# Optimization experiments

Measured on AMD Instinct MI355X. Metric: run time of the kernel, lower is better.

The kernel has to match this reference:

```python
import jax, jax.numpy as jnp
import numpy as np

N, E, F_IN, GCH, H, HID, NOUT, NG = 5000, 15000, 300, 2048, 4, 2048, 768, 128
NEG_SLOPE = 0.2


def gat_conv(x, W, att_src, att_dst, bias, src, dst):
    # x: [N, Fin]; W: [Fin, H*C]; att_*: [H, C]; bias: [H*C]
    n = x.shape[0]
    h = (x @ W).reshape(n, H, GCH)                      # [N,H,C]
    a_src = (h * att_src).sum(-1)                       # [N,H]
    a_dst = (h * att_dst).sum(-1)                       # [N,H]
    e = jax.nn.leaky_relu(a_src[src] + a_dst[dst], NEG_SLOPE)  # [E,H]
    m = jax.ops.segment_max(e, dst, num_segments=n)     # segment softmax over dst
    e = jnp.exp(e - m[dst])
    s = jax.ops.segment_sum(e, dst, num_segments=n)
    alpha = e / (s[dst] + 1e-16)                        # [E,H]
    msg = h[src] * alpha[:, :, None]                    # [E,H,C]
    out = jax.ops.segment_sum(msg, dst, num_segments=n) # [N,H,C]
    return out.reshape(n, H * GCH) + bias


def setup_inputs() -> dict:
    key = jax.random.key(0)
    ks = jax.random.split(key, 32)
    d = {}
    d['x'] = jax.random.normal(ks[0], (N, F_IN), jnp.float32)
    d['edge_index'] = jax.random.randint(ks[1], (2, E), 0, N, jnp.int32)
    d['batch'] = jnp.sort(jax.random.randint(ks[2], (N,), 0, NG, jnp.int32))
    dims_in = [F_IN, HID, HID]
    i = 3
    for l, fin in enumerate(dims_in, 1):
        sc = 1.0 / np.sqrt(fin)
        d[f'W{l}'] = jax.random.normal(ks[i], (fin, H * GCH), jnp.float32) * sc; i += 1
        d[f'asrc{l}'] = jax.random.normal(ks[i], (H, GCH), jnp.float32) * 0.02; i += 1
        d[f'adst{l}'] = jax.random.normal(ks[i], (H, GCH), jnp.float32) * 0.02; i += 1
        d[f'bc{l}'] = jnp.zeros((H * GCH,), jnp.float32)
        d[f'Wh{l}'] = jax.random.normal(ks[i], (H * GCH, HID), jnp.float32) * (1.0 / np.sqrt(H * GCH)); i += 1
        d[f'bh{l}'] = jnp.zeros((HID,), jnp.float32)
    d['Wm1'] = jax.random.normal(ks[i], (GCH, 2048), jnp.float32) * (1.0 / np.sqrt(GCH)); i += 1
    d['bm1'] = jnp.zeros((2048,), jnp.float32)
    d['Wm2'] = jax.random.normal(ks[i], (2048, NOUT), jnp.float32) * (1.0 / np.sqrt(2048)); i += 1
    d['bm2'] = jnp.zeros((NOUT,), jnp.float32)
    d['ln_g'] = jnp.ones((NOUT,), jnp.float32)
    d['ln_b'] = jnp.zeros((NOUT,), jnp.float32)
    return d


def reference(x, edge_index, batch,
              W1, asrc1, adst1, bc1, Wh1, bh1,
              W2, asrc2, adst2, bc2, Wh2, bh2,
              W3, asrc3, adst3, bc3, Wh3, bh3,
              Wm1, bm1, Wm2, bm2, ln_g, ln_b):
    n = x.shape[0]
    # PyG GATConv adds self-loops by default
    loops = jnp.arange(n, dtype=edge_index.dtype)
    src = jnp.concatenate([edge_index[0], loops])
    dst = jnp.concatenate([edge_index[1], loops])

    h = gat_conv(x, W1, asrc1, adst1, bc1, src, dst)
    h = jax.nn.relu(h @ Wh1 + bh1)
    h = gat_conv(h, W2, asrc2, adst2, bc2, src, dst)
    h = jax.nn.relu(h @ Wh2 + bh2)
    h = gat_conv(h, W3, asrc3, adst3, bc3, src, dst)
    h = h @ Wh3 + bh3                                   # no relu after head_linear3

    # global mean pool over graphs
    sums = jax.ops.segment_sum(h, batch, num_segments=NG)
    cnt = jax.ops.segment_sum(jnp.ones((n,), h.dtype), batch, num_segments=NG)
    g = sums / jnp.maximum(cnt, 1.0)[:, None]           # [NG, 2048]

    g = jax.nn.relu(g @ Wm1 + bm1)
    g = g @ Wm2 + bm2                                   # [NG, NOUT]
    mu = g.mean(-1, keepdims=True)
    var = ((g - mu) ** 2).mean(-1, keepdims=True)
    return (g - mu) / jnp.sqrt(var + 1e-5) * ln_g + ln_b
```

## Files before the change

kernel.cpp:

```cpp
#include <hip/hip_runtime.h>

typedef unsigned short u16;
typedef __attribute__((ext_vector_type(8))) short short8;
typedef __attribute__((ext_vector_type(4))) short s16x4;
typedef __attribute__((ext_vector_type(4))) float f32x4;

__device__ inline u16 f2bf(float f){
  unsigned int u = __builtin_bit_cast(unsigned int, f);
  u += 0x7fffu + ((u >> 16) & 1u);
  return (u16)(u >> 16);
}
__device__ inline float bf2f(u16 h){
  unsigned int u = ((unsigned int)h) << 16;
  return __builtin_bit_cast(float, u);
}

typedef __attribute__((address_space(1))) const void* as1_t;
typedef __attribute__((address_space(3))) void* as3_t;
__device__ __forceinline__ void gload16(const u16* g, u16* l) {
  __builtin_amdgcn_global_load_lds((as1_t)g, (as3_t)l, 16, 0, 0);
}

#define BARRIER() asm volatile("s_barrier" ::: "memory")
#define VMCNT4()  asm volatile("s_waitcnt vmcnt(4)" ::: "memory")
#define VMCNT0()  asm volatile("s_waitcnt vmcnt(0)" ::: "memory")
#define LGKM0()   asm volatile("s_waitcnt lgkmcnt(0)" ::: "memory")

__device__ __forceinline__ void gemm_core(
    const u16* __restrict__ A, const u16* __restrict__ B, u16* __restrict__ C,
    int tile_m, int tile_n, int abase, int hoff,
    int M, int K, int lda, int ldb, int ldc, u16* lds)
{
  int tid = threadIdx.x, wave = tid >> 6, lane = tid & 63;
  int wm = wave >> 2, wn = wave & 3;
  int NT = K >> 6;

  const u16* sA[2]; const u16* sB[2];
  int dq[2];
#pragma unroll
  for (int q = 0; q < 2; ++q) {
    int row = q * 128 + (tid >> 2);
    int cg  = (tid & 3) ^ ((row >> 1) & 3);
    sA[q] = A + (size_t)(abase + row) * lda + hoff + cg * 8;
    sB[q] = B + (size_t)(tile_n + row) * ldb + hoff + cg * 8;
    dq[q] = q * 4096 + tid * 8;
  }

  int l15 = lane & 15, c4 = lane >> 4;
  int aoff[8], boff[4];
#pragma unroll
  for (int mi = 0; mi < 8; ++mi) {
    int r = wm * 128 + mi * 16 + l15;
    aoff[mi] = r * 32 + ((c4 ^ ((r >> 1) & 3)) * 8);
  }
#pragma unroll
  for (int ni = 0; ni < 4; ++ni) {
    int r = wn * 64 + ni * 16 + l15;
    boff[ni] = r * 32 + ((c4 ^ ((r >> 1) & 3)) * 8);
  }

  f32x4 acc[8][4];
#pragma unroll
  for (int mi = 0; mi < 8; ++mi)
#pragma unroll
    for (int ni = 0; ni < 4; ++ni) { f32x4 z = {0.f,0.f,0.f,0.f}; acc[mi][ni] = z; }

#define DSRA(fa, mb, base) \
  fa[0] = *reinterpret_cast<const short8*>(&lds[(base) + aoff[(mb)+0]]); \
  fa[1] = *reinterpret_cast<const short8*>(&lds[(base) + aoff[(mb)+1]]); \
  fa[2] = *reinterpret_cast<const short8*>(&lds[(base) + aoff[(mb)+2]]); \
  fa[3] = *reinterpret_cast<const short8*>(&lds[(base) + aoff[(mb)+3]]);
#define DSRB(fb, base) \
  fb[0] = *reinterpret_cast<const short8*>(&lds[(base) + boff[0]]); \
  fb[1] = *reinterpret_cast<const short8*>(&lds[(base) + boff[1]]); \
  fb[2] = *reinterpret_cast<const short8*>(&lds[(base) + boff[2]]); \
  fb[3] = *reinterpret_cast<const short8*>(&lds[(base) + boff[3]]);
#define MM16(mb, fa, fb) \
  _Pragma("unroll") for (int mi = 0; mi < 4; ++mi) \
  _Pragma("unroll") for (int ni = 0; ni < 4; ++ni) \
    acc[(mb)+mi][ni] = __builtin_amdgcn_mfma_f32_16x16x32_bf16(fa[mi], fb[ni], acc[(mb)+mi][ni], 0, 0, 0);
#define PH_SYNC() BARRIER(); LGKM0(); __builtin_amdgcn_sched_barrier(0)
#define PRIO1() __builtin_amdgcn_s_setprio(1)
#define PRIO0() __builtin_amdgcn_s_setprio(0)

#pragma unroll
  for (int q = 0; q < 2; ++q) {
    gload16(sA[q],      &lds[0     + dq[q]]);
    gload16(sB[q],      &lds[16384 + dq[q]]);
    gload16(sA[q] + 32, &lds[8192  + dq[q]]);
    gload16(sB[q] + 32, &lds[24576 + dq[q]]);
  }
  VMCNT0();
  BARRIER();

  for (int t = 0; t < NT; ++t) {
    int cb = (t & 1) * 32768;
    int nb = cb ^ 32768;
    bool st = (t + 1) < NT;
    int ke = (t + 1) * 64;
    short8 fa[4], fb0[4], fb1[4];
    DSRA(fa, 0, cb + 0);
    DSRB(fb0, cb + 16384);
    if (st) { gload16(sA[0] + ke, &lds[nb + dq[0]]);
              gload16(sA[1] + ke, &lds[nb + dq[1]]); }
    PH_SYNC(); PRIO1(); MM16(0, fa, fb0); PRIO0();
    BARRIER();
    DSRA(fa, 4, cb + 0);
    if (st) { gload16(sB[0] + ke, &lds[nb + 16384 + dq[0]]);
              gload16(sB[1] + ke, &lds[nb + 16384 + dq[1]]); }
    PH_SYNC(); PRIO1(); MM16(4, fa, fb0); PRIO0();
    if (st) { VMCNT4(); } else { VMCNT0(); }
    BARRIER();
    DSRA(fa, 0, cb + 8192);
    DSRB(fb1, cb + 24576);
    if (st) { gload16(sA[0] + ke + 32, &lds[nb + 8192 + dq[0]]);
              gload16(sA[1] + ke + 32, &lds[nb + 8192 + dq[1]]); }
    PH_SYNC(); PRIO1(); MM16(0, fa, fb1); PRIO0();
    BARRIER();
    DSRA(fa, 4, cb + 8192);
    if (st) { gload16(sB[0] + ke + 32, &lds[nb + 24576 + dq[0]]);
              gload16(sB[1] + ke + 32, &lds[nb + 24576 + dq[1]]); }
    PH_SYNC(); PRIO1(); MM16(4, fa, fb1); PRIO0();
    if (st) { VMCNT4(); }
    BARRIER();
  }

  int rq = (lane >> 4) * 4;
#pragma unroll
  for (int mi = 0; mi < 8; ++mi)
#pragma unroll
    for (int ni = 0; ni < 4; ++ni) {
      int col = tile_n + wn * 64 + ni * 16 + l15;
#pragma unroll
      for (int j = 0; j < 4; ++j) {
        int row = tile_m + wm * 128 + mi * 16 + rq + j;
        if (row < M) C[(size_t)row * ldc + col] = f2bf(acc[mi][ni][j]);
      }
    }
#undef DSRA
#undef DSRB
#undef MM16
#undef PH_SYNC
#undef PRIO1
#undef PRIO0
}

__global__ __launch_bounds__(512, 2) void gemm8p(
    const u16* __restrict__ A, const u16* __restrict__ B, u16* __restrict__ C,
    int M, int N, int K, int lda, int ldb, int ldc, int headed)
{
  __shared__ alignas(16) u16 lds[65536];
  int tile_m = blockIdx.y * 256, tile_n = blockIdx.x * 256;
  int hoff  = headed ? ((tile_m >> 11) << 11) : 0;
  int abase = headed ? (tile_m & 2047) : tile_m;
  gemm_core(A, B, C, tile_m, tile_n, abase, hoff, M, K, lda, ldb, ldc, lds);
}

__global__ __launch_bounds__(256) void prep_w(
    const float* __restrict__ W, u16* __restrict__ Wb,
    const float* __restrict__ asrc, const float* __restrict__ adst,
    float* __restrict__ wsd, int Fin, int Fp)
{
  int f = blockIdx.x;
  int w = threadIdx.x >> 6, lane = threadIdx.x & 63;
  if (f >= Fin) {
    s16x4 z = {0,0,0,0};
#pragma unroll
    for (int i = 0; i < 8; ++i)
      *reinterpret_cast<s16x4*>(Wb + (size_t)f * 8192 + w * 2048 + lane * 4 + i * 256) = z;
    if (lane == 0) { wsd[w * Fp + f] = 0.f; wsd[(4 + w) * Fp + f] = 0.f; }
    return;
  }
  const float* wr = W + (size_t)f * 8192 + w * 2048;
  const float* as = asrc + w * 2048;
  const float* ad = adst + w * 2048;
  u16* wb = Wb + (size_t)f * 8192 + w * 2048;
  float ss = 0.f, dd = 0.f;
#pragma unroll
  for (int i = 0; i < 8; ++i) {
    int c = lane * 4 + i * 256;
    f32x4 wv = *reinterpret_cast<const f32x4*>(wr + c);
    f32x4 av = *reinterpret_cast<const f32x4*>(as + c);
    f32x4 dv = *reinterpret_cast<const f32x4*>(ad + c);
    s16x4 ov;
#pragma unroll
    for (int j = 0; j < 4; ++j) {
      ss += wv[j] * av[j]; dd += wv[j] * dv[j];
      ov[j] = (short)f2bf(wv[j]);
    }
    *reinterpret_cast<s16x4*>(wb + c) = ov;
  }
  for (int off = 32; off; off >>= 1) {
    ss += __shfl_down(ss, off);
    dd += __shfl_down(dd, off);
  }
  if (lane == 0) { wsd[w * Fp + f] = ss; wsd[(4 + w) * Fp + f] = dd; }
}

__global__ __launch_bounds__(256) void transpose_bias(
    const float* __restrict__ Wh, u16* __restrict__ Wht,
    const float* __restrict__ bc, float* __restrict__ bhp)
{
  __shared__ float tile[32][33];
  int k0 = blockIdx.x * 32, n0 = blockIdx.y * 32;
  int tx = threadIdx.x & 31, ty = threadIdx.x >> 5;
#pragma unroll
  for (int i = 0; i < 4; ++i)
    tile[ty + i * 8][tx] = Wh[(size_t)(k0 + ty + i * 8) * 2048 + n0 + tx];
  __syncthreads();
#pragma unroll
  for (int i = 0; i < 4; ++i)
    Wht[(size_t)(n0 + ty + i * 8) * 8192 + k0 + tx] = f2bf(tile[tx][ty + i * 8]);
  if (threadIdx.x < 32) {
    float p = 0.f;
#pragma unroll
    for (int kk = 0; kk < 32; ++kk) p += bc[k0 + kk] * tile[kk][threadIdx.x];
    atomicAdd(&bhp[n0 + threadIdx.x], p);
  }
}

__global__ void init_bhp(const float* b0, const float* b1, const float* b2,
                         float* bhp){
  int i = blockIdx.x * 256 + threadIdx.x;
  int l = blockIdx.y;
  if (i < 2048) {
    const float* s = (l == 0) ? b0 : (l == 1 ? b1 : b2);
    bhp[l * 2048 + i] = s[i];
  }
}

__global__ __launch_bounds__(256) void transpose_cast(
    const float* __restrict__ W, u16* __restrict__ Wt, int K, int N, int Kpad)
{
  __shared__ float tile[32][33];
  int k0 = blockIdx.x * 32, n0 = blockIdx.y * 32;
  int tx = threadIdx.x & 31, ty = threadIdx.x >> 5;
#pragma unroll
  for (int i = 0; i < 4; ++i) {
    int k = k0 + ty + i * 8;
    float v = 0.f;
    if (k < K && (n0 + tx) < N) v = W[(size_t)k * N + n0 + tx];
    tile[ty + i * 8][tx] = v;
  }
  __syncthreads();
#pragma unroll
  for (int i = 0; i < 4; ++i) {
    int nn = n0 + ty + i * 8;
    if (nn < N) Wt[(size_t)nn * Kpad + k0 + tx] = f2bf(tile[tx][ty + i * 8]);
  }
}

__global__ void cast_pad(const float* __restrict__ x, u16* __restrict__ xb,
                         int R, int C, int Cp)
{
  int i = blockIdx.x * 256 + threadIdx.x;
  if (i >= R * Cp) return;
  int r = i / Cp, c = i % Cp;
  xb[i] = f2bf(c < C ? x[(size_t)r * C + c] : 0.f);
}

__global__ __launch_bounds__(256) void a_score(
    const u16* __restrict__ xb, const float* __restrict__ wsd,
    float* __restrict__ a_s, float* __restrict__ a_d, int Fp)
{
  int n = blockIdx.x, tid = threadIdx.x, lane = tid & 63, w = tid >> 6;
  float s[4] = {0.f,0.f,0.f,0.f}, d[4] = {0.f,0.f,0.f,0.f};
  int f = tid * 8;
  if (f < Fp) {
    short8 v = *reinterpret_cast<const short8*>(xb + (size_t)n * Fp + f);
#pragma unroll
    for (int j = 0; j < 8; ++j) {
      float xv = bf2f((u16)v[j]);
#pragma unroll
      for (int h = 0; h < 4; ++h) {
        s[h] += xv * wsd[h * Fp + f + j];
        d[h] += xv * wsd[(4 + h) * Fp + f + j];
      }
    }
  }
  __shared__ float red[4][8];
#pragma unroll
  for (int h = 0; h < 4; ++h) {
    for (int off = 32; off; off >>= 1) {
      s[h] += __shfl_down(s[h], off);
      d[h] += __shfl_down(d[h], off);
    }
  }
  if (lane == 0) {
#pragma unroll
    for (int h = 0; h < 4; ++h) { red[w][h] = s[h]; red[w][4 + h] = d[h]; }
  }
  __syncthreads();
  if (tid < 8) {
    float t = red[0][tid] + red[1][tid] + red[2][tid] + red[3][tid];
    if (tid < 4) a_s[n * 4 + tid] = t;
    else         a_d[n * 4 + tid - 4] = t;
  }
}

__global__ void zero_int(int* p, int n){ int i = blockIdx.x*256+threadIdx.x; if (i < n) p[i] = 0; }

__global__ void count_deg(const int* __restrict__ ei, int E, int Nn, int* __restrict__ deg){
  int e = blockIdx.x*256+threadIdx.x; if (e >= E + Nn) return;
  int d = (e < E) ? ei[E + e] : (e - E);
  atomicAdd(&deg[d], 1);
}

__global__ void scan_deg(const int* __restrict__ deg, int* __restrict__ row_st,
                         int* __restrict__ cursor, int Nn){
  __shared__ int partial[256];
  int tid = threadIdx.x;
  int chunk = (Nn + 255) / 256;
  int start = tid * chunk;
  int sum = 0;
  for (int i = 0; i < chunk; ++i) { int idx = start + i; if (idx < Nn) sum += deg[idx]; }
  partial[tid] = sum;
  __syncthreads();
  if (tid == 0) { int acc = 0; for (int i = 0; i < 256; ++i) { int t = partial[i]; partial[i] = acc; acc += t; } }
  __syncthreads();
  int acc = partial[tid];
  for (int i = 0; i < chunk; ++i) {
    int idx = start + i;
    if (idx < Nn) { row_st[idx] = acc; cursor[idx] = acc; acc += deg[idx]; }
  }
  if (tid == 255) row_st[Nn] = acc;
}

__global__ void scatter_edges(const int* __restrict__ ei, int E, int Nn,
                              int* __restrict__ cursor, int* __restrict__ srcs){
  int e = blockIdx.x*256+threadIdx.x; if (e >= E + Nn) return;
  int s = (e < E) ? ei[e]     : (e - E);
  int d = (e < E) ? ei[E + e] : (e - E);
  int pos = atomicAdd(&cursor[d], 1);
  srcs[pos] = s;
}

__global__ void edge_softmax(const int* __restrict__ row_st, const int* __restrict__ srcs,
                             const float* __restrict__ a_s, const float* __restrict__ a_d,
                             float* __restrict__ alpha, int Nn){
  int t = blockIdx.x*256+threadIdx.x;
  if (t >= Nn * 4) return;
  int n = t >> 2, hh = t & 3;
  int b = row_st[n], e = row_st[n + 1];
  float ad = a_d[n * 4 + hh];
  float m = -1e30f;
  for (int p = b; p < e; ++p) {
    float x = a_s[srcs[p] * 4 + hh] + ad;
    x = x > 0.f ? x : 0.2f * x;
    alpha[p * 4 + hh] = x;
    m = fmaxf(m, x);
  }
  float ssum = 0.f;
  for (int p = b; p < e; ++p) {
    float ex = expf(alpha[p * 4 + hh] - m);
    alpha[p * 4 + hh] = ex;
    ssum += ex;
  }
  float inv = 1.f / (ssum + 1e-16f);
  for (int p = b; p < e; ++p) alpha[p * 4 + hh] *= inv;
}

__global__ __launch_bounds__(256) void aggregate2(
    const u16* __restrict__ z, const float* __restrict__ alpha,
    const int* __restrict__ row_st, const int* __restrict__ srcs,
    const float* __restrict__ bhp, u16* __restrict__ out, int relu,
    const float* __restrict__ wsd_next, float* __restrict__ psum)
{
  int n = blockIdx.x, half = blockIdx.y, tid = threadIdx.x;
  int c = half * 1024 + tid * 4;
  float acc[4] = {0.f, 0.f, 0.f, 0.f};
  int b = row_st[n], e = row_st[n + 1];

  int s0 = srcs[b];
  const u16* zr = z + (size_t)s0 * 8192 + c;
  s16x4 v0 = *reinterpret_cast<const s16x4*>(zr);
  s16x4 v1 = *reinterpret_cast<const s16x4*>(zr + 2048);
  s16x4 v2 = *reinterpret_cast<const s16x4*>(zr + 4096);
  s16x4 v3 = *reinterpret_cast<const s16x4*>(zr + 6144);
  float a0 = alpha[b * 4 + 0], a1 = alpha[b * 4 + 1];
  float a2 = alpha[b * 4 + 2], a3 = alpha[b * 4 + 3];

  for (int p = b; p < e; ++p) {
    s16x4 w0 = v0, w1 = v1, w2 = v2, w3 = v3;
    float b0 = a0, b1 = a1, b2 = a2, b3 = a3;
    if (p + 1 < e) {
      int s1 = srcs[p + 1];
      const u16* zr2 = z + (size_t)s1 * 8192 + c;
      v0 = *reinterpret_cast<const s16x4*>(zr2);
      v1 = *reinterpret_cast<const s16x4*>(zr2 + 2048);
      v2 = *reinterpret_cast<const s16x4*>(zr2 + 4096);
      v3 = *reinterpret_cast<const s16x4*>(zr2 + 6144);
      a0 = alpha[(p + 1) * 4 + 0]; a1 = alpha[(p + 1) * 4 + 1];
      a2 = alpha[(p + 1) * 4 + 2]; a3 = alpha[(p + 1) * 4 + 3];
    }
#pragma unroll
    for (int q = 0; q < 4; ++q)
      acc[q] += b0 * bf2f((u16)w0[q]) + b1 * bf2f((u16)w1[q])
              + b2 * bf2f((u16)w2[q]) + b3 * bf2f((u16)w3[q]);
  }

  float sv[4] = {0.f,0.f,0.f,0.f}, dv[4] = {0.f,0.f,0.f,0.f};
  s16x4 ov;
#pragma unroll
  for (int q = 0; q < 4; ++q) {
    float v = acc[q] + bhp[c + q];
    if (relu) v = fmaxf(v, 0.f);
    ov[q] = (short)f2bf(v);
    if (wsd_next) {
#pragma unroll
      for (int h = 0; h < 4; ++h) {
        sv[h] += v * wsd_next[h * 2048 + c + q];
        dv[h] += v * wsd_next[(4 + h) * 2048 + c + q];
      }
    }
  }
  *reinterpret_cast<s16x4*>(out + (size_t)n * 2048 + c) = ov;
  if (wsd_next) {
    int lane = tid & 63, w = tid >> 6;
    __shared__ float red[4][8];
#pragma unroll
    for (int h = 0; h < 4; ++h) {
      for (int off = 32; off; off >>= 1) {
        sv[h] += __shfl_down(sv[h], off);
        dv[h] += __shfl_down(dv[h], off);
      }
    }
    if (lane == 0) {
#pragma unroll
      for (int h = 0; h < 4; ++h) { red[w][h] = sv[h]; red[w][4 + h] = dv[h]; }
    }
    __syncthreads();
    if (tid < 8) {
      float t = red[0][tid] + red[1][tid] + red[2][tid] + red[3][tid];
      psum[(size_t)n * 16 + half * 8 + tid] = t;
    }
  }
}

__global__ void combine_scores(const float* __restrict__ psum,
                               float* __restrict__ a_s, float* __restrict__ a_d,
                               int Nn){
  int i = blockIdx.x * 256 + threadIdx.x;
  if (i >= Nn * 4) return;
  int n = i >> 2, h = i & 3;
  a_s[i] = psum[(size_t)n * 16 + h]     + psum[(size_t)n * 16 + 8 + h];
  a_d[i] = psum[(size_t)n * 16 + 4 + h] + psum[(size_t)n * 16 + 12 + h];
}

__global__ __launch_bounds__(256) void pool_mean(
    const u16* __restrict__ hf, const int* __restrict__ batch,
    u16* __restrict__ g, int Nn)
{
  int gid = blockIdx.x, tid = threadIdx.x;
  int s1, s2;
  { int l = 0, h = Nn; while (l < h) { int m = (l + h) >> 1; if (batch[m] < gid) l = m + 1; else h = m; } s1 = l; }
  { int l = 0, h = Nn; while (l < h) { int m = (l + h) >> 1; if (batch[m] < gid + 1) l = m + 1; else h = m; } s2 = l; }
  float inv = 1.f / fmaxf((float)(s2 - s1), 1.f);
  float acc[8];
#pragma unroll
  for (int q = 0; q < 8; ++q) acc[q] = 0.f;
  for (int r = s1; r < s2; ++r) {
    short8 v = *reinterpret_cast<const short8*>(hf + (size_t)r * 2048 + tid * 8);
#pragma unroll
    for (int q = 0; q < 8; ++q) acc[q] += bf2f((u16)v[q]);
  }
  short8 ov;
#pragma unroll
  for (int q = 0; q < 8; ++q) ov[q] = (short)f2bf(acc[q] * inv);
  *reinterpret_cast<short8*>(g + (size_t)gid * 2048 + tid * 8) = ov;
}

__global__ __launch_bounds__(256) void gemm_bt(
    const u16* __restrict__ A, const u16* __restrict__ B,
    float* __restrict__ Cf, u16* __restrict__ Cb,
    const float* __restrict__ bias, int M, int N, int K, int relu)
{
  __shared__ alignas(16) u16 As[128 * 32];
  __shared__ alignas(16) u16 Bs[128 * 32];
  int tid = threadIdx.x;
  int wave = tid >> 6, lane = tid & 63;
  int wr = wave >> 1, wc = wave & 1;
  int tile_m = blockIdx.y * 128, tile_n = blockIdx.x * 128;

  int sr = wave * 16 + (lane >> 2);
  int sc = (lane & 3) * 8;
  const u16* gA0 = A + (size_t)(tile_m + sr) * K + sc;
  const u16* gA1 = A + (size_t)(tile_m + 64 + sr) * K + sc;
  const u16* gB0 = B + (size_t)(tile_n + sr) * K + sc;
  const u16* gB1 = B + (size_t)(tile_n + 64 + sr) * K + sc;
  u16* lA0 = &As[wave * 512];
  u16* lA1 = &As[2048 + wave * 512];
  u16* lB0 = &Bs[wave * 512];
  u16* lB1 = &Bs[2048 + wave * 512];

  f32x4 acc[4][4];
#pragma unroll
  for (int mi = 0; mi < 4; ++mi)
#pragma unroll
    for (int ni = 0; ni < 4; ++ni) { f32x4 z = {0.f,0.f,0.f,0.f}; acc[mi][ni] = z; }

  int lrow = lane & 15, lk = (lane >> 4) * 8;

  for (int k0 = 0; k0 < K; k0 += 32) {
    gload16(gA0 + k0, lA0);
    gload16(gA1 + k0, lA1);
    gload16(gB0 + k0, lB0);
    gload16(gB1 + k0, lB1);
    __syncthreads();
    short8 af[4], bfr[4];
#pragma unroll
    for (int mi = 0; mi < 4; ++mi)
      af[mi] = *reinterpret_cast<const short8*>(&As[(wr * 64 + mi * 16 + lrow) * 32 + lk]);
#pragma unroll
    for (int ni = 0; ni < 4; ++ni)
      bfr[ni] = *reinterpret_cast<const short8*>(&Bs[(wc * 64 + ni * 16 + lrow) * 32 + lk]);
#pragma unroll
    for (int mi = 0; mi < 4; ++mi)
#pragma unroll
      for (int ni = 0; ni < 4; ++ni)
        acc[mi][ni] = __builtin_amdgcn_mfma_f32_16x16x32_bf16(af[mi], bfr[ni], acc[mi][ni], 0, 0, 0);
    __syncthreads();
  }

  int rquad = (lane >> 4) * 4;
#pragma unroll
  for (int mi = 0; mi < 4; ++mi)
#pragma unroll
    for (int ni = 0; ni < 4; ++ni) {
      int col = tile_n + wc * 64 + ni * 16 + lrow;
      float bv = bias ? bias[col] : 0.f;
#pragma unroll
      for (int j = 0; j < 4; ++j) {
        int row = tile_m + wr * 64 + mi * 16 + rquad + j;
        if (row < M) {
          float v = acc[mi][ni][j] + bv;
          if (relu) v = fmaxf(v, 0.f);
          if (Cb) Cb[(size_t)row * N + col] = f2bf(v);
          else    Cf[(size_t)row * N + col] = v;
        }
      }
    }
}

__global__ __launch_bounds__(256) void layernorm_768(
    const float* __restrict__ x, const float* __restrict__ gam,
    const float* __restrict__ bet, float* __restrict__ out)
{
  int row = blockIdx.x, tid = threadIdx.x, lane = tid & 63, w = tid >> 6;
  __shared__ float sh[8];
  float v0 = x[row * 768 + tid];
  float v1 = x[row * 768 + 256 + tid];
  float v2 = x[row * 768 + 512 + tid];
  float s = v0 + v1 + v2;
  for (int off = 32; off; off >>= 1) s += __shfl_down(s, off);
  if (lane == 0) sh[w] = s;
  __syncthreads();
  if (tid == 0) sh[4] = (sh[0] + sh[1] + sh[2] + sh[3]) / 768.f;
  __syncthreads();
  float mu = sh[4];
  float d0 = v0 - mu, d1 = v1 - mu, d2 = v2 - mu;
  float q = d0 * d0 + d1 * d1 + d2 * d2;
  for (int off = 32; off; off >>= 1) q += __shfl_down(q, off);
  if (lane == 0) sh[w] = q;
  __syncthreads();
  if (tid == 0) sh[5] = rsqrtf((sh[0] + sh[1] + sh[2] + sh[3]) / 768.f + 1e-5f);
  __syncthreads();
  float rstd = sh[5];
  out[row * 768 + tid]       = d0 * rstd * gam[tid]       + bet[tid];
  out[row * 768 + 256 + tid] = d1 * rstd * gam[256 + tid] + bet[256 + tid];
  out[row * 768 + 512 + tid] = d2 * rstd * gam[512 + tid] + bet[512 + tid];
}

extern "C" void kernel_launch(void* const* d_in, const int* in_sizes, int n_in,
                              void* d_out, int out_size, void* d_ws, size_t ws_size,
                              hipStream_t stream)
{
  const float* x     = (const float*)d_in[0];
  const int*   ei    = (const int*)d_in[1];
  const int*   batch = (const int*)d_in[2];
  const float* W[3]   = {(const float*)d_in[3], (const float*)d_in[9],  (const float*)d_in[15]};
  const float* asr[3] = {(const float*)d_in[4], (const float*)d_in[10], (const float*)d_in[16]};
  const float* ads[3] = {(const float*)d_in[5], (const float*)d_in[11], (const float*)d_in[17]};
  const float* bc[3]  = {(const float*)d_in[6], (const float*)d_in[12], (const float*)d_in[18]};
  const float* Wh[3]  = {(const float*)d_in[7], (const float*)d_in[13], (const float*)d_in[19]};
  const float* bh[3]  = {(const float*)d_in[8], (const float*)d_in[14], (const float*)d_in[20]};
  const float* Wm1 = (const float*)d_in[21];
  const float* bm1 = (const float*)d_in[22];
  const float* Wm2 = (const float*)d_in[23];
  const float* bm2 = (const float*)d_in[24];
  const float* lng = (const float*)d_in[25];
  const float* lnb = (const float*)d_in[26];
  float* out = (float*)d_out;

  int Nn = in_sizes[2];
  int E  = in_sizes[1] / 2;
  int ET = E + Nn;

  char* base = (char*)d_ws;
  size_t off = 0;
  auto alloc = [&](size_t b) -> char* { char* p = base + off; off = (off + b + 255) & ~(size_t)255; return p; };
  u16*  actA  = (u16*)alloc((size_t)5120 * 2048 * 2);
  u16*  actB  = (u16*)alloc((size_t)5120 * 2048 * 2);
  u16*  Ut0   = (u16*)alloc((size_t)8192 * 512  * 2);
  u16*  Ut1   = (u16*)alloc((size_t)8192 * 2048 * 2);
  u16*  Ut2   = (u16*)alloc((size_t)8192 * 2048 * 2);
  u16*  zb    = (u16*)alloc((size_t)5120 * 8192 * 2);
  u16*  xb0   = (u16*)alloc((size_t)5120 * 512 * 2);
  float* wsd  = (float*)alloc((size_t)3 * 8 * 2048 * 4);
  float* bhp  = (float*)alloc((size_t)3 * 2048 * 4);
  float* a_s  = (float*)alloc((size_t)Nn * 4 * 4);
  float* a_d  = (float*)alloc((size_t)Nn * 4 * 4);
  float* psum = (float*)alloc((size_t)Nn * 16 * 4);
  float* alpha= (float*)alloc((size_t)ET * 4 * 4);
  int*  deg   = (int*)alloc((size_t)(Nn + 1) * 4);
  int*  rowst = (int*)alloc((size_t)(Nn + 1) * 4);
  int*  cursor= (int*)alloc((size_t)(Nn + 1) * 4);
  int*  srcs  = (int*)alloc((size_t)ET * 4);
  u16*  g     = (u16*)alloc((size_t)128 * 2048 * 2);
  u16*  g2    = (u16*)alloc((size_t)128 * 2048 * 2);
  float* preln= (float*)alloc((size_t)128 * 768 * 4);

  u16* Wb_sh  = zb;
  u16* Wht_sh = zb + (size_t)2048 * 8192;

  zero_int<<<(Nn + 255) / 256, 256, 0, stream>>>(deg, Nn);
  count_deg<<<(ET + 255) / 256, 256, 0, stream>>>(ei, E, Nn, deg);
  scan_deg<<<1, 256, 0, stream>>>(deg, rowst, cursor, Nn);
  scatter_edges<<<(ET + 255) / 256, 256, 0, stream>>>(ei, E, Nn, cursor, srcs);
  cast_pad<<<(Nn * 512 + 255) / 256, 256, 0, stream>>>(x, xb0, Nn, 300, 512);

  init_bhp<<<dim3(8, 3), 256, 0, stream>>>(bh[0], bh[1], bh[2], bhp);
  prep_w<<<512, 256, 0, stream>>>(W[0], Wb_sh, asr[0], ads[0], wsd, 300, 512);
  transpose_bias<<<dim3(256, 64), 256, 0, stream>>>(Wh[0], Wht_sh, bc[0], bhp);
  gemm8p<<<dim3(2, 32), 512, 0, stream>>>(Wht_sh, Wb_sh, Ut0, 8192, 512, 2048, 8192, 8192, 512, 1);
  prep_w<<<2048, 256, 0, stream>>>(W[1], Wb_sh, asr[1], ads[1], wsd + 16384, 2048, 2048);
  transpose_bias<<<dim3(256, 64), 256, 0, stream>>>(Wh[1], Wht_sh, bc[1], bhp + 2048);
  gemm8p<<<dim3(8, 32), 512, 0, stream>>>(Wht_sh, Wb_sh, Ut1, 8192, 2048, 2048, 8192, 8192, 2048, 1);
  prep_w<<<2048, 256, 0, stream>>>(W[2], Wb_sh, asr[2], ads[2], wsd + 32768, 2048, 2048);
  transpose_bias<<<dim3(256, 64), 256, 0, stream>>>(Wh[2], Wht_sh, bc[2], bhp + 4096);
  gemm8p<<<dim3(8, 32), 512, 0, stream>>>(Wht_sh, Wb_sh, Ut2, 8192, 2048, 2048, 8192, 8192, 2048, 1);

  a_score<<<Nn, 256, 0, stream>>>(xb0, wsd, a_s, a_d, 512);

  const u16* act = xb0;
  u16* Ut[3] = {Ut0, Ut1, Ut2};
  for (int l = 0; l < 3; ++l) {
    int Fp = (l == 0) ? 512 : 2048;
    u16* outb = (l & 1) ? actB : actA;
    edge_softmax<<<(Nn * 4 + 255) / 256, 256, 0, stream>>>(rowst, srcs, a_s, a_d, alpha, Nn);
    gemm8p<<<dim3(32, 20), 512, 0, stream>>>(act, Ut[l], zb, Nn, 8192, Fp, Fp, Fp, 8192, 0);
    aggregate2<<<dim3(Nn, 2), 256, 0, stream>>>(zb, alpha, rowst, srcs, bhp + l * 2048, outb,
                                                (l < 2) ? 1 : 0,
                                                (l < 2) ? (wsd + (l + 1) * 16384) : nullptr,
                                                psum);
    if (l < 2)
      combine_scores<<<(Nn * 4 + 255) / 256, 256, 0, stream>>>(psum, a_s, a_d, Nn);
    act = outb;
  }

  pool_mean<<<128, 256, 0, stream>>>(act, batch, g, Nn);
  u16* Mt1 = zb;
  u16* Mt2 = zb + (size_t)2048 * 2048;
  transpose_cast<<<dim3(64, 64), 256, 0, stream>>>(Wm1, Mt1, 2048, 2048, 2048);
  gemm_bt<<<dim3(16, 1), 256, 0, stream>>>(g, Mt1, nullptr, g2, bm1, 128, 2048, 2048, 1);
  transpose_cast<<<dim3(64, 24), 256, 0, stream>>>(Wm2, Mt2, 2048, 768, 2048);
  gemm_bt<<<dim3(6, 1), 256, 0, stream>>>(g2, Mt2, preln, nullptr, bm2, 128, 768, 2048, 0);
  layernorm_768<<<128, 256, 0, stream>>>(preln, lng, lnb, out);
}
```

Measured before the change: 1.244 ms.

## Merge layer-0/1 weight-product GEMMs into one launch; deepen aggregate prefetch

Layer-0 weights get their own buffers, so the layer-0 and layer-1 weight-product GEMMs (64 and 256 tiles) run as a single 320-block launch. This fills the GPU better than two separate small launches. The aggregation kernel now prefetches two edges ahead instead of one, hiding more gather latency at the cost of extra registers. The two ping-pong activation buffers are merged into one, which is safe because the GEMM reads the activation before aggregate overwrites it.

```diff
diff --git a/kernel.cpp b/kernel.cpp
--- a/kernel.cpp
+++ b/kernel.cpp
@@ -156,6 +156,25 @@
   gemm_core(A, B, C, tile_m, tile_n, abase, hoff, M, K, lda, ldb, ldc, lds);
 }
 
+__global__ __launch_bounds__(512, 2) void gemm8p_u2(
+    const u16* A0, const u16* B0, u16* C0, int N0,
+    const u16* A1, const u16* B1, u16* C1, int N1, int s1)
+{
+  __shared__ alignas(16) u16 lds[65536];
+  int flat = blockIdx.x;
+  int j = flat >= s1;
+  const u16* A = j ? A1 : A0;
+  const u16* B = j ? B1 : B0;
+  u16*       C = j ? C1 : C0;
+  int N = j ? N1 : N0;
+  int lbx = flat - (j ? s1 : 0);
+  int ntile = N >> 8;
+  int tile_n = (lbx % ntile) * 256;
+  int tile_m = (lbx / ntile) * 256;
+  gemm_core(A, B, C, tile_m, tile_n, tile_m & 2047, (tile_m >> 11) << 11,
+            8192, 2048, 8192, 8192, N, lds);
+}
+
 __global__ __launch_bounds__(256) void prep_w(
     const float* __restrict__ W, u16* __restrict__ Wb,
     const float* __restrict__ asrc, const float* __restrict__ adst,
@@ -373,25 +392,39 @@
 
   int s0 = srcs[b];
   const u16* zr = z + (size_t)s0 * 8192 + c;
-  s16x4 v0 = *reinterpret_cast<const s16x4*>(zr);
-  s16x4 v1 = *reinterpret_cast<const s16x4*>(zr + 2048);
-  s16x4 v2 = *reinterpret_cast<const s16x4*>(zr + 4096);
-  s16x4 v3 = *reinterpret_cast<const s16x4*>(zr + 6144);
-  float a0 = alpha[b * 4 + 0], a1 = alpha[b * 4 + 1];
-  float a2 = alpha[b * 4 + 2], a3 = alpha[b * 4 + 3];
+  s16x4 cv0 = *reinterpret_cast<const s16x4*>(zr);
+  s16x4 cv1 = *reinterpret_cast<const s16x4*>(zr + 2048);
+  s16x4 cv2 = *reinterpret_cast<const s16x4*>(zr + 4096);
+  s16x4 cv3 = *reinterpret_cast<const s16x4*>(zr + 6144);
+  float ca0 = alpha[b * 4 + 0], ca1 = alpha[b * 4 + 1];
+  float ca2 = alpha[b * 4 + 2], ca3 = alpha[b * 4 + 3];
+  s16x4 nv0, nv1, nv2, nv3;
+  float na0 = 0.f, na1 = 0.f, na2 = 0.f, na3 = 0.f;
+  if (b + 1 < e) {
+    int s1 = srcs[b + 1];
+    const u16* zr1 = z + (size_t)s1 * 8192 + c;
+    nv0 = *reinterpret_cast<const s16x4*>(zr1);
+    nv1 = *reinterpret_cast<const s16x4*>(zr1 + 2048);
+    nv2 = *reinterpret_cast<const s16x4*>(zr1 + 4096);
+    nv3 = *reinterpret_cast<const s16x4*>(zr1 + 6144);
+    na0 = alpha[(b + 1) * 4 + 0]; na1 = alpha[(b + 1) * 4 + 1];
+    na2 = alpha[(b + 1) * 4 + 2]; na3 = alpha[(b + 1) * 4 + 3];
+  }
 
   for (int p = b; p < e; ++p) {
-    s16x4 w0 = v0, w1 = v1, w2 = v2, w3 = v3;
-    float b0 = a0, b1 = a1, b2 = a2, b3 = a3;
-    if (p + 1 < e) {
-      int s1 = srcs[p + 1];
-      const u16* zr2 = z + (size_t)s1 * 8192 + c;
-      v0 = *reinterpret_cast<const s16x4*>(zr2);
-      v1 = *reinterpret_cast<const s16x4*>(zr2 + 2048);
-      v2 = *reinterpret_cast<const s16x4*>(zr2 + 4096);
-      v3 = *reinterpret_cast<const s16x4*>(zr2 + 6144);
-      a0 = alpha[(p + 1) * 4 + 0]; a1 = alpha[(p + 1) * 4 + 1];
-      a2 = alpha[(p + 1) * 4 + 2]; a3 = alpha[(p + 1) * 4 + 3];
+    s16x4 w0 = cv0, w1 = cv1, w2 = cv2, w3 = cv3;
+    float b0 = ca0, b1 = ca1, b2 = ca2, b3 = ca3;
+    cv0 = nv0; cv1 = nv1; cv2 = nv2; cv3 = nv3;
+    ca0 = na0; ca1 = na1; ca2 = na2; ca3 = na3;
+    if (p + 2 < e) {
+      int s2 = srcs[p + 2];
+      const u16* zr2 = z + (size_t)s2 * 8192 + c;
+      nv0 = *reinterpret_cast<const s16x4*>(zr2);
+      nv1 = *reinterpret_cast<const s16x4*>(zr2 + 2048);
+      nv2 = *reinterpret_cast<const s16x4*>(zr2 + 4096);
+      nv3 = *reinterpret_cast<const s16x4*>(zr2 + 6144);
+      na0 = alpha[(p + 2) * 4 + 0]; na1 = alpha[(p + 2) * 4 + 1];
+      na2 = alpha[(p + 2) * 4 + 2]; na3 = alpha[(p + 2) * 4 + 3];
     }
 #pragma unroll
     for (int q = 0; q < 4; ++q)
@@ -599,8 +632,9 @@
   char* base = (char*)d_ws;
   size_t off = 0;
   auto alloc = [&](size_t b) -> char* { char* p = base + off; off = (off + b + 255) & ~(size_t)255; return p; };
-  u16*  actA  = (u16*)alloc((size_t)5120 * 2048 * 2);
-  u16*  actB  = (u16*)alloc((size_t)5120 * 2048 * 2);
+  u16*  act   = (u16*)alloc((size_t)5120 * 2048 * 2);
+  u16*  Wb0d  = (u16*)alloc((size_t)512  * 8192 * 2);
+  u16*  Wht0d = (u16*)alloc((size_t)2048 * 8192 * 2);
   u16*  Ut0   = (u16*)alloc((size_t)8192 * 512  * 2);
   u16*  Ut1   = (u16*)alloc((size_t)8192 * 2048 * 2);
   u16*  Ut2   = (u16*)alloc((size_t)8192 * 2048 * 2);
@@ -630,32 +664,31 @@
   cast_pad<<<(Nn * 512 + 255) / 256, 256, 0, stream>>>(x, xb0, Nn, 300, 512);
 
   init_bhp<<<dim3(8, 3), 256, 0, stream>>>(bh[0], bh[1], bh[2], bhp);
-  prep_w<<<512, 256, 0, stream>>>(W[0], Wb_sh, asr[0], ads[0], wsd, 300, 512);
-  transpose_bias<<<dim3(256, 64), 256, 0, stream>>>(Wh[0], Wht_sh, bc[0], bhp);
-  gemm8p<<<dim3(2, 32), 512, 0, stream>>>(Wht_sh, Wb_sh, Ut0, 8192, 512, 2048, 8192, 8192, 512, 1);
+  prep_w<<<512, 256, 0, stream>>>(W[0], Wb0d, asr[0], ads[0], wsd, 300, 512);
+  transpose_bias<<<dim3(256, 64), 256, 0, stream>>>(Wh[0], Wht0d, bc[0], bhp);
   prep_w<<<2048, 256, 0, stream>>>(W[1], Wb_sh, asr[1], ads[1], wsd + 16384, 2048, 2048);
   transpose_bias<<<dim3(256, 64), 256, 0, stream>>>(Wh[1], Wht_sh, bc[1], bhp + 2048);
-  gemm8p<<<dim3(8, 32), 512, 0, stream>>>(Wht_sh, Wb_sh, Ut1, 8192, 2048, 2048, 8192, 8192, 2048, 1);
+  gemm8p_u2<<<320, 512, 0, stream>>>(Wht0d, Wb0d, Ut0, 512,
+                                     Wht_sh, Wb_sh, Ut1, 2048, 64);
   prep_w<<<2048, 256, 0, stream>>>(W[2], Wb_sh, asr[2], ads[2], wsd + 32768, 2048, 2048);
   transpose_bias<<<dim3(256, 64), 256, 0, stream>>>(Wh[2], Wht_sh, bc[2], bhp + 4096);
   gemm8p<<<dim3(8, 32), 512, 0, stream>>>(Wht_sh, Wb_sh, Ut2, 8192, 2048, 2048, 8192, 8192, 2048, 1);
 
   a_score<<<Nn, 256, 0, stream>>>(xb0, wsd, a_s, a_d, 512);
 
-  const u16* act = xb0;
+  const u16* actcur = xb0;
   u16* Ut[3] = {Ut0, Ut1, Ut2};
   for (int l = 0; l < 3; ++l) {
     int Fp = (l == 0) ? 512 : 2048;
-    u16* outb = (l & 1) ? actB : actA;
     edge_softmax<<<(Nn * 4 + 255) / 256, 256, 0, stream>>>(rowst, srcs, a_s, a_d, alpha, Nn);
-    gemm8p<<<dim3(32, 20), 512, 0, stream>>>(act, Ut[l], zb, Nn, 8192, Fp, Fp, Fp, 8192, 0);
-    aggregate2<<<dim3(Nn, 2), 256, 0, stream>>>(zb, alpha, rowst, srcs, bhp + l * 2048, outb,
+    gemm8p<<<dim3(32, 20), 512, 0, stream>>>(actcur, Ut[l], zb, Nn, 8192, Fp, Fp, Fp, 8192, 0);
+    aggregate2<<<dim3(Nn, 2), 256, 0, stream>>>(zb, alpha, rowst, srcs, bhp + l * 2048, act,
                                                 (l < 2) ? 1 : 0,
                                                 (l < 2) ? (wsd + (l + 1) * 16384) : nullptr,
                                                 psum);
     if (l < 2)
       combine_scores<<<(Nn * 4 + 255) / 256, 256, 0, stream>>>(psum, a_s, a_d, Nn);
-    act = outb;
+    actcur = act;
   }
 
   pool_mean<<<128, 256, 0, stream>>>(act, batch, g, Nn);
```

Measured after the change: 1.249 ms. About the same (+0.4%).
